# Kernel tuning notes

Measured on AMD Instinct MI355X. Metric: run time of the kernel, lower is better.

## Reference

```python
import jax, jax.numpy as jnp
import numpy as np

M_MARGIN = 0.25
GAMMA = 64.0
EPS = 1e-5


def _circle_loss_one_way(enc, dec):
    # enc, dec: [N, D]. Faithful to the torch rotate-concat construction:
    # cos_sim[j, k] = cosine(enc[j], dec[(j + k) % N]); column 0 is the positive.
    N = enc.shape[0]
    dot = enc @ dec.T                                   # [N, N]
    en = jnp.sqrt(jnp.sum(enc * enc, axis=1, keepdims=True))   # [N, 1]
    dn = jnp.sqrt(jnp.sum(dec * dec, axis=1, keepdims=True))   # [N, 1]
    S = dot / (en * dn.T + EPS)                         # [N, N] cosine sims
    r = jnp.arange(N)
    idx = (r[:, None] + r[None, :]) % N                 # [N, N] rolled column index
    cos_sim = jnp.take_along_axis(S, idx, axis=1)       # [N, N]
    sp = cos_sim[:, 0:1]                                # [N, 1] positives (diag of S)
    sn = cos_sim[:, 1:]                                 # [N, N-1] negatives
    ap = jnp.maximum(-jax.lax.stop_gradient(sp) + 1.0 + M_MARGIN, 0.0)
    an = jnp.maximum(jax.lax.stop_gradient(sn) + M_MARGIN, 0.0)
    delta_p = 1.0 - M_MARGIN
    delta_n = M_MARGIN
    logit_p = -ap * (sp - delta_p) * GAMMA              # [N, 1]
    logit_n = an * (sn - delta_n) * GAMMA               # [N, N-1]
    lse_n = jax.nn.logsumexp(logit_n, axis=0)           # [N-1]
    lse_p = jax.nn.logsumexp(logit_p, axis=0)           # [1] (cols of repeated sp are identical)
    return jax.nn.softplus(lse_n + lse_p)               # [N-1]


def reference(encoder_output, decoder_output):
    loss_a = _circle_loss_one_way(encoder_output, decoder_output)
    loss_b = _circle_loss_one_way(decoder_output, encoder_output)
    return jnp.mean((loss_a + loss_b) / 2.0)


def setup_inputs() -> dict:
    key = jax.random.key(0)
    k1, k2 = jax.random.split(key)
    N, D = 8192, 128
    return {
        "encoder_output": jax.random.normal(k1, (N, D), dtype=jnp.float32),
        "decoder_output": jax.random.normal(k2, (N, D), dtype=jnp.float32),
    }
```

## Files before the change

### kernel.cpp

```cpp
#include <hip/hip_runtime.h>
#include <hip/hip_bf16.h>

#define NN 8192

using f32x4 = __attribute__((ext_vector_type(4))) float;
using i32x4v = __attribute__((ext_vector_type(4))) int;
using i32x8v = __attribute__((ext_vector_type(8))) int;

#if __has_builtin(__builtin_amdgcn_exp2f)
#define EXP2(x) __builtin_amdgcn_exp2f(x)
#else
#define EXP2(x) __expf((x) * 0.69314718056f)
#endif

__device__ __forceinline__ void gl_lds16(const void* g, void* l) {
  __builtin_amdgcn_global_load_lds(
      (const __attribute__((address_space(1))) unsigned int*)(unsigned long long)g,
      (__attribute__((address_space(3))) unsigned int*)(unsigned int)(unsigned long long)l,
      16, 0, 0);
}

#if __has_builtin(__builtin_amdgcn_cvt_pk_fp8_f32)
__device__ __forceinline__ unsigned pk4_fp8(float x0, float x1, float x2, float x3) {
  unsigned w = (unsigned)__builtin_amdgcn_cvt_pk_fp8_f32(x0, x1, 0, false);
  w = (unsigned)__builtin_amdgcn_cvt_pk_fp8_f32(x2, x3, (int)w, true);
  return w;
}
#else
__device__ __forceinline__ unsigned f8_1(float f) {
  unsigned u = __float_as_uint(f);
  unsigned s = (u >> 24) & 0x80u;
  float a = fabsf(f);
  if (a < 0.015625f) {
    unsigned m = (unsigned)rintf(a * 512.0f);
    return s | (m > 7u ? 8u : m);
  }
  if (a > 448.0f) return s | 0x7Eu;
  unsigned au = u & 0x7FFFFFFFu;
  unsigned e = (au >> 23) - 127u + 7u;
  unsigned m23 = au & 0x7FFFFFu;
  unsigned m = m23 >> 20;
  unsigned rem = m23 & 0xFFFFFu;
  if (rem > 0x80000u || (rem == 0x80000u && (m & 1u))) {
    if (++m == 8u) { m = 0u; ++e; }
  }
  return s | (e << 3) | m;
}
__device__ __forceinline__ unsigned pk4_fp8(float x0, float x1, float x2, float x3) {
  return f8_1(x0) | (f8_1(x1) << 8) | (f8_1(x2) << 16) | (f8_1(x3) << 24);
}
#endif

__global__ __launch_bounds__(256) void k_prep(const float* __restrict__ enc,
                                              const float* __restrict__ dec,
                                              uint2* __restrict__ A8,
                                              uint2* __restrict__ B8,
                                              float* __restrict__ logit_p,
                                              float* __restrict__ bandsum,
                                              unsigned* __restrict__ counter) {
  const int t = threadIdx.x;
  const int l16 = t & 15;
  const int row = blockIdx.x * 16 + (t >> 4);
  const int tid = blockIdx.x * 256 + t;
  if (tid < 64 * 256) bandsum[tid] = 0.0f;
  if (tid == 64 * 256) *counter = 0u;

  const float4* e4 = reinterpret_cast<const float4*>(enc) + (size_t)row * 32 + l16 * 2;
  const float4* d4 = reinterpret_cast<const float4*>(dec) + (size_t)row * 32 + l16 * 2;
  float4 e0 = e4[0], e1 = e4[1];
  float4 d0 = d4[0], d1 = d4[1];

  float se = e0.x*e0.x + e0.y*e0.y + e0.z*e0.z + e0.w*e0.w
           + e1.x*e1.x + e1.y*e1.y + e1.z*e1.z + e1.w*e1.w;
  float sd = d0.x*d0.x + d0.y*d0.y + d0.z*d0.z + d0.w*d0.w
           + d1.x*d1.x + d1.y*d1.y + d1.z*d1.z + d1.w*d1.w;
  float sp = e0.x*d0.x + e0.y*d0.y + e0.z*d0.z + e0.w*d0.w
           + e1.x*d1.x + e1.y*d1.y + e1.z*d1.z + e1.w*d1.w;
#pragma unroll
  for (int off = 1; off < 16; off <<= 1) {
    se += __shfl_xor(se, off);
    sd += __shfl_xor(sd, off);
    sp += __shfl_xor(sp, off);
  }
  float ie = rsqrtf(se), id = rsqrtf(sd);

  uint2 ua, ub;
  ua.x = pk4_fp8(e0.x * ie, e0.y * ie, e0.z * ie, e0.w * ie);
  ua.y = pk4_fp8(e1.x * ie, e1.y * ie, e1.z * ie, e1.w * ie);
  ub.x = pk4_fp8(d0.x * id, d0.y * id, d0.z * id, d0.w * id);
  ub.y = pk4_fp8(d1.x * id, d1.y * id, d1.z * id, d1.w * id);
  A8[(size_t)row * 16 + l16] = ua;
  B8[(size_t)row * 16 + l16] = ub;

  if (l16 == 0) {
    float en = se * ie, dn = sd * id;
    float s  = sp / (en * dn + 1e-5f);
    logit_p[row] = -fmaxf(1.25f - s, 0.0f) * (s - 0.75f) * 64.0f;
  }
}

__device__ __forceinline__ i32x8v ld_frag32(const unsigned char* __restrict__ buf,
                                            int rowbase, int q2, int x7) {
  i32x4v lo = *reinterpret_cast<const i32x4v*>(buf + rowbase + ((q2 ^ x7) * 16));
  i32x4v hi = *reinterpret_cast<const i32x4v*>(buf + rowbase + (((q2 + 1) ^ x7) * 16));
  i32x8v r;
  r[0] = lo[0]; r[1] = lo[1]; r[2] = lo[2]; r[3] = lo[3];
  r[4] = hi[0]; r[5] = hi[1]; r[6] = hi[2]; r[7] = hi[3];
  return r;
}

__device__ __forceinline__ void epi(const f32x4 (&acc)[4][4], float (&dreg)[28]) {
#pragma unroll
  for (int dlt = -3; dlt <= 3; ++dlt) {
#pragma unroll
    for (int g = 0; g < 4; ++g) {
      float s = 0.0f;
#pragma unroll
      for (int r = 0; r < 4; ++r) {
        int c = r + dlt;
        if (c < 0 || c > 3) continue;
        float x  = fmaxf(acc[r][c][g], -0.25f);
        float wv = x * 9.6089793f;
        s += EXP2(fmaf(wv, wv, -5.7707802f));
      }
      dreg[(dlt + 3) * 4 + g] += s;
    }
  }
}

__global__ __launch_bounds__(256, 2) void k_main(const unsigned char* __restrict__ A,
                                                 const unsigned char* __restrict__ B,
                                                 float* __restrict__ bandsum,
                                                 const float* __restrict__ logit_p,
                                                 unsigned* __restrict__ counter,
                                                 float* __restrict__ out) {
  __shared__ __align__(16) unsigned char As[2 * 16384];
  __shared__ __align__(16) unsigned char Bs[2 * 16384];
  __shared__ float part[4][256];
  __shared__ unsigned lastFlag;

  const int t  = threadIdx.x;
  const int T  = blockIdx.x;
  const int sp = blockIdx.y;

#pragma unroll
  for (int q = 0; q < 4; ++q) part[q][t] = 0.0f;

  const int lane = t & 63;
  const int w = t >> 6, wrow = w >> 1, wcol = w & 1;
  const int l15 = lane & 15, quad = lane >> 4;
  const int x7 = l15 & 7;
  const int q2 = quad * 2;
#if !__has_builtin(__builtin_amdgcn_mfma_scale_f32_16x16x128_f8f6f4)
  const int qh = quad >> 1, ql8 = (quad & 1) * 8;
#endif

  const int rl = t >> 3;
  const int lgoff = rl * 128 + ((t & 7) ^ (rl & 7)) * 16;
  const int lloff = t * 16;

  const char* Ab = (const char*)A;
  const char* Bb = (const char*)B;

  float dreg[28];
#pragma unroll
  for (int i = 0; i < 28; ++i) dreg[i] = 0.0f;

  const int arow = (wrow * 64 + l15) * 128;
  const int brow = (wcol * 64 + l15) * 128;

  {
    const int by = sp * 8;
    const int bx = (by + T) & 63;
    const char* Ag = Ab + (size_t)by * 16384 + lgoff;
    const char* Bg = Bb + (size_t)bx * 16384 + lgoff;
#pragma unroll
    for (int j = 0; j < 4; ++j) {
      gl_lds16(Ag + j * 4096, (char*)As + j * 4096 + lloff);
      gl_lds16(Bg + j * 4096, (char*)Bs + j * 4096 + lloff);
    }
  }
  __syncthreads();

  const f32x4 zv4 = {0.f, 0.f, 0.f, 0.f};
  f32x4 acc[4][4];

  for (int it = 0; it < 8; ++it) {
    const int p = it & 1;

    if (it < 7) {
      const int by = sp * 8 + it + 1;
      const int bx = (by + T) & 63;
      const char* Ag = Ab + (size_t)by * 16384 + lgoff;
      const char* Bg = Bb + (size_t)bx * 16384 + lgoff;
      char* Ad = (char*)As + (p ^ 1) * 16384 + lloff;
      char* Bd = (char*)Bs + (p ^ 1) * 16384 + lloff;
#pragma unroll
      for (int j = 0; j < 4; ++j) {
        gl_lds16(Ag + j * 4096, Ad + j * 4096);
        gl_lds16(Bg + j * 4096, Bd + j * 4096);
      }
    }

    const unsigned char* Abuf = (const unsigned char*)As + p * 16384;
    const unsigned char* Bbuf = (const unsigned char*)Bs + p * 16384;

#if __has_builtin(__builtin_amdgcn_mfma_scale_f32_16x16x128_f8f6f4)
    i32x8v af[4], bf[4];
#pragma unroll
    for (int c = 0; c < 4; ++c) bf[c] = ld_frag32(Bbuf, brow + c * 2048, q2, x7);
#pragma unroll
    for (int r = 0; r < 4; ++r) af[r] = ld_frag32(Abuf, arow + r * 2048, q2, x7);

    if (it) epi(acc, dreg);

    __builtin_amdgcn_s_setprio(1);
#pragma unroll
    for (int r = 0; r < 4; ++r)
#pragma unroll
      for (int c = 0; c < 4; ++c)
        acc[r][c] = __builtin_amdgcn_mfma_scale_f32_16x16x128_f8f6f4(
            af[r], bf[c], zv4, 0, 0,
            0, 0x7F7F7F7F, 0, 0x7F7F7F7F);
    __builtin_amdgcn_s_setprio(0);
#else
    {
      if (it) epi(acc, dreg);
      const f32x4 zv = {0.f, 0.f, 0.f, 0.f};
#pragma unroll
      for (int r = 0; r < 4; ++r)
#pragma unroll
        for (int c = 0; c < 4; ++c) acc[r][c] = zv;
#pragma unroll
      for (int ks = 0; ks < 4; ++ks) {
        long a[4], b[4];
        const int off = (((ks * 2 + qh) ^ x7) * 16) + ql8;
#pragma unroll
        for (int r = 0; r < 4; ++r)
          a[r] = *reinterpret_cast<const long*>(Abuf + arow + r * 2048 + off);
#pragma unroll
        for (int c = 0; c < 4; ++c)
          b[c] = *reinterpret_cast<const long*>(Bbuf + brow + c * 2048 + off);
#pragma unroll
        for (int r = 0; r < 4; ++r)
#pragma unroll
          for (int c = 0; c < 4; ++c)
            acc[r][c] = __builtin_amdgcn_mfma_f32_16x16x32_fp8_fp8(a[r], b[c], acc[r][c], 0, 0, 0);
      }
    }
#endif

    __syncthreads();
  }

  epi(acc, dreg);

  const int  Qoff = (wcol - wrow) * 64 + 127;
  const int  v    = l15 - quad * 4;
  const bool leader = (quad == 0) || (l15 <= 3);
  const bool ok1 = (l15 <= 11) && (quad <= 2);
  const bool ok2 = (l15 <= 7)  && (quad <= 1);

#pragma unroll
  for (int dlt = -3; dlt <= 3; ++dlt) {
#pragma unroll
    for (int g = 0; g < 4; ++g) {
      float s = dreg[(dlt + 3) * 4 + g];
      float t1 = __shfl_down(s, 20); s += ok1 ? t1 : 0.0f;
      float t2 = __shfl_down(s, 40); s += ok2 ? t2 : 0.0f;
      int ld = Qoff + dlt * 16 - g + v;
      if (leader) unsafeAtomicAdd(&part[w][ld], s);
    }
  }
  __syncthreads();

  if (t < 255) {
    float vv = part[0][t] + part[1][t] + part[2][t] + part[3][t];
    unsafeAtomicAdd(&bandsum[T * 256 + t], vv);
  }

  __syncthreads();
  if (t == 0) lastFlag = (atomicAdd(counter, 1u) == 511u) ? 1u : 0u;
  __syncthreads();
  if (!lastFlag) return;

  __threadfence();
  float* sm = part[0];

  float lp[32];
#pragma unroll
  for (int k = 0; k < 32; ++k) lp[k] = logit_p[t + 256 * k];

  float m = lp[0];
#pragma unroll
  for (int k = 1; k < 32; ++k) m = fmaxf(m, lp[k]);
#pragma unroll
  for (int off = 32; off; off >>= 1) m = fmaxf(m, __shfl_down(m, off));
  if (lane == 0) sm[w] = m;
  __syncthreads();
  m = fmaxf(fmaxf(sm[0], sm[1]), fmaxf(sm[2], sm[3]));
  __syncthreads();

  float s = 0.0f;
#pragma unroll
  for (int k = 0; k < 32; ++k) s += __expf(lp[k] - m);
#pragma unroll
  for (int off = 32; off; off >>= 1) s += __shfl_down(s, off);
  if (lane == 0) sm[w] = s;
  __syncthreads();
  s = sm[0] + sm[1] + sm[2] + sm[3];
  float lse_p = m + __logf(s);
  __syncthreads();

  const int o  = t & 127;
  const int hi = t >> 7;
  float bs1[32], bs2[32];
#pragma unroll
  for (int k = 0; k < 32; ++k) {
    int Ta = hi + 2 * k;
    bs1[k] = bandsum[Ta * 256 + o + 127];
    bs2[k] = o ? bandsum[((Ta + 1) & 63) * 256 + o - 1] : 0.0f;
  }
  float tacc = 0.0f;
#pragma unroll
  for (int k = 0; k < 32; ++k) {
    if (t == 0 && k == 0) continue;
    float se = bs1[k] + bs2[k];
    float x = __logf(se) + lse_p;
    tacc += fmaxf(x, 0.0f) + __logf(1.0f + __expf(-fabsf(x)));
  }
#pragma unroll
  for (int off = 32; off; off >>= 1) tacc += __shfl_down(tacc, off);
  if (lane == 0) sm[w] = tacc;
  __syncthreads();
  if (t == 0) out[0] = (sm[0] + sm[1] + sm[2] + sm[3]) * (1.0f / 8191.0f);
}

extern "C" void kernel_launch(void* const* d_in, const int* in_sizes, int n_in,
                              void* d_out, int out_size, void* d_ws, size_t ws_size,
                              hipStream_t stream) {
  const float* enc = (const float*)d_in[0];
  const float* dec = (const float*)d_in[1];
  float* ws = (float*)d_ws;

  float*    logit_p = ws;
  float*    bandsum = ws + 8192;
  unsigned* counter = (unsigned*)(ws + 8192 + 16384);
  uint2*    A8      = (uint2*)(ws + 8192 + 16384 + 256);
  uint2*    B8      = (uint2*)((char*)A8 + 1048576);
  float*    out     = (float*)d_out;

  k_prep<<<NN / 16, 256, 0, stream>>>(enc, dec, A8, B8, logit_p, bandsum, counter);
  dim3 grid(64, 8);
  k_main<<<grid, 256, 0, stream>>>((const unsigned char*)A8, (const unsigned char*)B8,
                                   bandsum, logit_p, counter, out);
}
```

Baseline: 92.72 us.

## Fuse prep into main kernel with a grid-wide spin barrier

Folds the normalization/FP8 quantization prep pass into the main GEMM+epilogue kernel. Each block converts 16 rows, then all blocks wait on a global atomic counter before the main phase begins. A tiny init kernel resets the counters. This aims to remove the launch gap and tail between the two kernels. In exchange it relies on all 512 blocks being co-resident, or the spin barrier deadlocks, and it still pays for an extra small launch.

New measurement: 133.5 us. 44.0% more time.

```diff
diff --git a/kernel.cpp b/kernel.cpp
--- a/kernel.cpp
+++ b/kernel.cpp
@@ -51,54 +51,6 @@
 }
 #endif
 
-__global__ __launch_bounds__(256) void k_prep(const float* __restrict__ enc,
-                                              const float* __restrict__ dec,
-                                              uint2* __restrict__ A8,
-                                              uint2* __restrict__ B8,
-                                              float* __restrict__ logit_p,
-                                              float* __restrict__ bandsum,
-                                              unsigned* __restrict__ counter) {
-  const int t = threadIdx.x;
-  const int l16 = t & 15;
-  const int row = blockIdx.x * 16 + (t >> 4);
-  const int tid = blockIdx.x * 256 + t;
-  if (tid < 64 * 256) bandsum[tid] = 0.0f;
-  if (tid == 64 * 256) *counter = 0u;
-
-  const float4* e4 = reinterpret_cast<const float4*>(enc) + (size_t)row * 32 + l16 * 2;
-  const float4* d4 = reinterpret_cast<const float4*>(dec) + (size_t)row * 32 + l16 * 2;
-  float4 e0 = e4[0], e1 = e4[1];
-  float4 d0 = d4[0], d1 = d4[1];
-
-  float se = e0.x*e0.x + e0.y*e0.y + e0.z*e0.z + e0.w*e0.w
-           + e1.x*e1.x + e1.y*e1.y + e1.z*e1.z + e1.w*e1.w;
-  float sd = d0.x*d0.x + d0.y*d0.y + d0.z*d0.z + d0.w*d0.w
-           + d1.x*d1.x + d1.y*d1.y + d1.z*d1.z + d1.w*d1.w;
-  float sp = e0.x*d0.x + e0.y*d0.y + e0.z*d0.z + e0.w*d0.w
-           + e1.x*d1.x + e1.y*d1.y + e1.z*d1.z + e1.w*d1.w;
-#pragma unroll
-  for (int off = 1; off < 16; off <<= 1) {
-    se += __shfl_xor(se, off);
-    sd += __shfl_xor(sd, off);
-    sp += __shfl_xor(sp, off);
-  }
-  float ie = rsqrtf(se), id = rsqrtf(sd);
-
-  uint2 ua, ub;
-  ua.x = pk4_fp8(e0.x * ie, e0.y * ie, e0.z * ie, e0.w * ie);
-  ua.y = pk4_fp8(e1.x * ie, e1.y * ie, e1.z * ie, e1.w * ie);
-  ub.x = pk4_fp8(d0.x * id, d0.y * id, d0.z * id, d0.w * id);
-  ub.y = pk4_fp8(d1.x * id, d1.y * id, d1.z * id, d1.w * id);
-  A8[(size_t)row * 16 + l16] = ua;
-  B8[(size_t)row * 16 + l16] = ub;
-
-  if (l16 == 0) {
-    float en = se * ie, dn = sd * id;
-    float s  = sp / (en * dn + 1e-5f);
-    logit_p[row] = -fmaxf(1.25f - s, 0.0f) * (s - 0.75f) * 64.0f;
-  }
-}
-
 __device__ __forceinline__ i32x8v ld_frag32(const unsigned char* __restrict__ buf,
                                             int rowbase, int q2, int x7) {
   i32x4v lo = *reinterpret_cast<const i32x4v*>(buf + rowbase + ((q2 ^ x7) * 16));
@@ -128,20 +80,82 @@
   }
 }
 
-__global__ __launch_bounds__(256, 2) void k_main(const unsigned char* __restrict__ A,
-                                                 const unsigned char* __restrict__ B,
-                                                 float* __restrict__ bandsum,
-                                                 const float* __restrict__ logit_p,
-                                                 unsigned* __restrict__ counter,
-                                                 float* __restrict__ out) {
+__global__ __launch_bounds__(64) void k_init(unsigned* __restrict__ mainCnt,
+                                             unsigned* __restrict__ prepCnt) {
+  if (threadIdx.x == 0) {
+    atomicExch(mainCnt, 0u);
+    atomicExch(prepCnt, 0u);
+  }
+}
+
+__global__ __launch_bounds__(256, 2) void k_all(const float* __restrict__ enc,
+                                                const float* __restrict__ dec,
+                                                uint2* __restrict__ A8,
+                                                uint2* __restrict__ B8,
+                                                float* __restrict__ logit_p,
+                                                float* __restrict__ bandsum,
+                                                unsigned* __restrict__ mainCnt,
+                                                unsigned* __restrict__ prepCnt,
+                                                float* __restrict__ out) {
   __shared__ __align__(16) unsigned char As[2 * 16384];
   __shared__ __align__(16) unsigned char Bs[2 * 16384];
   __shared__ float part[4][256];
   __shared__ unsigned lastFlag;
 
-  const int t  = threadIdx.x;
-  const int T  = blockIdx.x;
-  const int sp = blockIdx.y;
+  const int t   = threadIdx.x;
+  const int T   = blockIdx.x;
+  const int sp  = blockIdx.y;
+  const int bid = sp * 64 + T;
+
+  {
+    const int l16 = t & 15;
+    const int row = bid * 16 + (t >> 4);
+    const int tid = bid * 256 + t;
+    if (tid < 64 * 256) bandsum[tid] = 0.0f;
+
+    const float4* e4 = reinterpret_cast<const float4*>(enc) + (size_t)row * 32 + l16 * 2;
+    const float4* d4 = reinterpret_cast<const float4*>(dec) + (size_t)row * 32 + l16 * 2;
+    float4 e0 = e4[0], e1 = e4[1];
+    float4 d0 = d4[0], d1 = d4[1];
+
+    float se = e0.x*e0.x + e0.y*e0.y + e0.z*e0.z + e0.w*e0.w
+             + e1.x*e1.x + e1.y*e1.y + e1.z*e1.z + e1.w*e1.w;
+    float sd = d0.x*d0.x + d0.y*d0.y + d0.z*d0.z + d0.w*d0.w
+             + d1.x*d1.x + d1.y*d1.y + d1.z*d1.z + d1.w*d1.w;
+    float sp_ = e0.x*d0.x + e0.y*d0.y + e0.z*d0.z + e0.w*d0.w
+              + e1.x*d1.x + e1.y*d1.y + e1.z*d1.z + e1.w*d1.w;
+#pragma unroll
+    for (int off = 1; off < 16; off <<= 1) {
+      se  += __shfl_xor(se, off);
+      sd  += __shfl_xor(sd, off);
+      sp_ += __shfl_xor(sp_, off);
+    }
+    float ie = rsqrtf(se), id = rsqrtf(sd);
+
+    uint2 ua, ub;
+    ua.x = pk4_fp8(e0.x * ie, e0.y * ie, e0.z * ie, e0.w * ie);
+    ua.y = pk4_fp8(e1.x * ie, e1.y * ie, e1.z * ie, e1.w * ie);
+    ub.x = pk4_fp8(d0.x * id, d0.y * id, d0.z * id, d0.w * id);
+    ub.y = pk4_fp8(d1.x * id, d1.y * id, d1.z * id, d1.w * id);
+    A8[(size_t)row * 16 + l16] = ua;
+    B8[(size_t)row * 16 + l16] = ub;
+
+    if (l16 == 0) {
+      float en = se * ie, dn = sd * id;
+      float s  = sp_ / (en * dn + 1e-5f);
+      logit_p[row] = -fmaxf(1.25f - s, 0.0f) * (s - 0.75f) * 64.0f;
+    }
+  }
+
+  __syncthreads();
+  if (t == 0) {
+    __threadfence();
+    atomicAdd(prepCnt, 1u);
+    while (__hip_atomic_load(prepCnt, __ATOMIC_RELAXED, __HIP_MEMORY_SCOPE_AGENT) < 512u)
+      __builtin_amdgcn_s_sleep(4);
+    __threadfence();
+  }
+  __syncthreads();
 
 #pragma unroll
   for (int q = 0; q < 4; ++q) part[q][t] = 0.0f;
@@ -159,8 +173,8 @@
   const int lgoff = rl * 128 + ((t & 7) ^ (rl & 7)) * 16;
   const int lloff = t * 16;
 
-  const char* Ab = (const char*)A;
-  const char* Bb = (const char*)B;
+  const char* Ab = (const char*)A8;
+  const char* Bb = (const char*)B8;
 
   float dreg[28];
 #pragma unroll
@@ -280,7 +294,7 @@
   }
 
   __syncthreads();
-  if (t == 0) lastFlag = (atomicAdd(counter, 1u) == 511u) ? 1u : 0u;
+  if (t == 0) lastFlag = (atomicAdd(mainCnt, 1u) == 511u) ? 1u : 0u;
   __syncthreads();
   if (!lastFlag) return;
 
@@ -345,13 +359,14 @@
 
   float*    logit_p = ws;
   float*    bandsum = ws + 8192;
-  unsigned* counter = (unsigned*)(ws + 8192 + 16384);
+  unsigned* mainCnt = (unsigned*)(ws + 8192 + 16384);
+  unsigned* prepCnt = (unsigned*)(ws + 8192 + 16384) + 1;
   uint2*    A8      = (uint2*)(ws + 8192 + 16384 + 256);
   uint2*    B8      = (uint2*)((char*)A8 + 1048576);
   float*    out     = (float*)d_out;
 
-  k_prep<<<NN / 16, 256, 0, stream>>>(enc, dec, A8, B8, logit_p, bandsum, counter);
+  k_init<<<1, 64, 0, stream>>>(mainCnt, prepCnt);
   dim3 grid(64, 8);
-  k_main<<<grid, 256, 0, stream>>>((const unsigned char*)A8, (const unsigned char*)B8,
-                                   bandsum, logit_p, counter, out);
-}
+  k_all<<<grid, 256, 0, stream>>>(enc, dec, A8, B8, logit_p, bandsum,
+                                  mainCnt, prepCnt, out);
+}
```
